# Performance work log

Hardware: AMD Instinct MI355X
Metric: run time of the kernel (lower is better)

The kernel has to match this reference:

```python
import jax, jax.numpy as jnp
import numpy as np

N_EMBEDS = 1024
N_HEADS = 16
HEAD_DIM = N_EMBEDS // N_HEADS
SCALE = HEAD_DIM ** (-0.5)
B, T = 2, 2048


def setup_inputs() -> dict:
    key = jax.random.key(0)
    k1, k2, k3, k4 = jax.random.split(key, 4)
    x = jax.random.normal(k1, (B, T, N_EMBEDS), dtype=jnp.float32)
    # Glorot-uniform-style init like keras Dense defaults (scale irrelevant for correctness)
    w_qkv = jax.random.normal(k2, (N_EMBEDS, 3 * N_EMBEDS), dtype=jnp.float32) * (N_EMBEDS ** -0.5)
    w_proj = jax.random.normal(k3, (N_EMBEDS, N_EMBEDS), dtype=jnp.float32) * (N_EMBEDS ** -0.5)
    b_proj = jnp.zeros((N_EMBEDS,), dtype=jnp.float32)
    return {"x": x, "w_qkv": w_qkv, "w_proj": w_proj, "b_proj": b_proj}


def reference(x, w_qkv, w_proj, b_proj):
    Bc, Tc, D = x.shape
    qkv = x @ w_qkv                                   # [B,T,3D]
    q, k, v = jnp.split(qkv, 3, axis=-1)
    def heads(t):
        return t.reshape(Bc, Tc, N_HEADS, HEAD_DIM).transpose(0, 2, 1, 3)  # [B,H,T,hd]
    q, k, v = heads(q), heads(k), heads(v)
    att = jnp.einsum("bhqd,bhkd->bhqk", q, k) * SCALE  # [B,H,T,T]
    causal = jnp.tril(jnp.ones((Tc, Tc), dtype=bool))[None, None]
    att = jnp.where(causal, att, jnp.float32(-1e9))
    att = jax.nn.softmax(att, axis=-1)
    out = jnp.einsum("bhqk,bhkd->bhqd", att, v)        # [B,H,T,hd]
    out = out.transpose(0, 2, 1, 3).reshape(Bc, Tc, D)
    return out @ w_proj + b_proj
```

## Files before the change

### kernel.cpp

```cpp
#include <hip/hip_runtime.h>
#include <hip/hip_bf16.h>


typedef __bf16 bf16;
typedef float f32x4 __attribute__((ext_vector_type(4)));
typedef float f32x16 __attribute__((ext_vector_type(16)));
typedef bf16 bf16x4 __attribute__((ext_vector_type(4)));
typedef bf16 bf16x8 __attribute__((ext_vector_type(8)));

#define B_ 2
#define T_ 2048
#define D_ 1024
#define H_ 16
#define HD_ 64
#define QSPLIT 9

__device__ __forceinline__ f32x16 mfma32(bf16x8 a, bf16x8 b, f32x16 c) {
    return __builtin_amdgcn_mfma_f32_32x32x16_bf16(a, b, c, 0, 0, 0);
}

__device__ __forceinline__ void gload16(void* l, const void* g) {
    __builtin_amdgcn_global_load_lds(
        (const __attribute__((address_space(1))) unsigned int*)g,
        (__attribute__((address_space(3))) unsigned int*)l, 16, 0, 0);
}

__device__ __forceinline__ f32x16 z16() {
    f32x16 v;
#pragma unroll
    for (int i = 0; i < 16; ++i) v[i] = 0.f;
    return v;
}

__global__ __launch_bounds__(256) void cast_f32_bf16(const float* __restrict__ in,
                                                     bf16* __restrict__ out, int n4) {
    int i = blockIdx.x * 256 + threadIdx.x;
    if (i < n4) {
        float4 v = ((const float4*)in)[i];
        bf16x4 o = { (bf16)v.x, (bf16)v.y, (bf16)v.z, (bf16)v.w };
        ((bf16x4*)out)[i] = o;
    }
}

__global__ __launch_bounds__(256) void cast_transpose(const float* __restrict__ in,
                                                      bf16* __restrict__ out, int R, int C) {
    __shared__ float tile[32][33];
    int cx = blockIdx.x * 32 + threadIdx.x;
    int r0 = blockIdx.y * 32;
#pragma unroll
    for (int j = 0; j < 32; j += 8)
        tile[threadIdx.y + j][threadIdx.x] = in[(size_t)(r0 + threadIdx.y + j) * C + cx];
    __syncthreads();
    int rx = r0 + threadIdx.x;
    int c0 = blockIdx.x * 32;
#pragma unroll
    for (int j = 0; j < 32; j += 8)
        out[(size_t)(c0 + threadIdx.y + j) * R + rx] = (bf16)tile[threadIdx.x][threadIdx.y + j];
}

__global__ __launch_bounds__(256) void transpose_v(const bf16* __restrict__ vb,
                                                   bf16* __restrict__ vt) {
    __shared__ bf16 st[64 * 65];
    const int bh = blockIdx.y;
    const int t0 = blockIdx.x * 64;
    const int tid = threadIdx.x;
#pragma unroll
    for (int c = 0; c < 2; ++c) {
        int cid = tid + c * 256;
        int r = cid >> 3, col = (cid & 7) * 8;
        bf16x8 v = *(const bf16x8*)&vb[((size_t)bh * T_ + t0 + r) * HD_ + col];
#pragma unroll
        for (int j = 0; j < 8; ++j) st[r * 65 + col + j] = v[j];
    }
    __syncthreads();
#pragma unroll
    for (int c = 0; c < 2; ++c) {
        int cid = tid + c * 256;
        int tg = cid & 7, d = cid >> 3;
        bf16x8 o;
#pragma unroll
        for (int j = 0; j < 8; ++j) o[j] = st[(tg * 8 + j) * 65 + d];
        *(bf16x8*)&vt[((size_t)bh * HD_ + d) * T_ + t0 + tg * 8] = o;
    }
}

template <int MW, int NWN, int EPI>
__global__ __launch_bounds__(256) void gemm_k(
    const bf16* __restrict__ A, const bf16* __restrict__ Bt,
    int M, int N, int K,
    bf16* __restrict__ qb, bf16* __restrict__ kb, bf16* __restrict__ vb,
    const float* __restrict__ bias, float* __restrict__ outf) {
    constexpr int BM = 64 * MW;
    constexpr int BN = 64 * NWN;
    __shared__ bf16 sA[BM * 64];
    __shared__ bf16 sB[BN * 64];
    const int tid = threadIdx.x;
    const int wave = tid >> 6, lane = tid & 63;
    const int ln = lane & 31, hi = lane >> 5;
    const int wr = (wave >> 1) * (32 * MW);
    const int wc = (wave & 1) * (32 * NWN);
    const int m0 = blockIdx.x * BM, n0 = blockIdx.y * BN;

    f32x16 acc[MW][NWN];
#pragma unroll
    for (int mi = 0; mi < MW; ++mi)
#pragma unroll
        for (int ni = 0; ni < NWN; ++ni) acc[mi][ni] = z16();

    for (int k0 = 0; k0 < K; k0 += 64) {
        __syncthreads();
#pragma unroll
        for (int j = 0; j < 2 * MW; ++j) {
            int c = tid + 256 * j;
            int r = c >> 3, g = (c & 7) ^ (r & 7);
            gload16(&sA[c * 8], A + (size_t)(m0 + r) * K + k0 + 8 * g);
        }
#pragma unroll
        for (int j = 0; j < 2 * NWN; ++j) {
            int c = tid + 256 * j;
            int r = c >> 3, g = (c & 7) ^ (r & 7);
            gload16(&sB[c * 8], Bt + (size_t)(n0 + r) * K + k0 + 8 * g);
        }
        __syncthreads();
#pragma unroll
        for (int s = 0; s < 4; ++s) {
            bf16x8 av[MW], bv[NWN];
#pragma unroll
            for (int mi = 0; mi < MW; ++mi) {
                int r = wr + mi * 32 + ln;
                av[mi] = *(const bf16x8*)((const char*)sA + r * 128 +
                                          ((((s << 1) | hi) ^ (r & 7)) << 4));
            }
#pragma unroll
            for (int ni = 0; ni < NWN; ++ni) {
                int r = wc + ni * 32 + ln;
                bv[ni] = *(const bf16x8*)((const char*)sB + r * 128 +
                                          ((((s << 1) | hi) ^ (r & 7)) << 4));
            }
#pragma unroll
            for (int mi = 0; mi < MW; ++mi)
#pragma unroll
                for (int ni = 0; ni < NWN; ++ni)
                    acc[mi][ni] = mfma32(av[mi], bv[ni], acc[mi][ni]);
        }
    }

#pragma unroll
    for (int mi = 0; mi < MW; ++mi)
#pragma unroll
        for (int ni = 0; ni < NWN; ++ni)
#pragma unroll
            for (int r = 0; r < 16; ++r) {
                int row = m0 + wr + mi * 32 + (r & 3) + 8 * (r >> 2) + 4 * hi;
                int col = n0 + wc + ni * 32 + ln;
                float v = acc[mi][ni][r];
                if (EPI == 0) {
                    int part = col >> 10, h = (col >> 6) & 15, d = col & 63;
                    int b = row >> 11, t = row & (T_ - 1);
                    size_t idx = ((size_t)(b * H_ + h) * T_ + t) * HD_ + d;
                    bf16* dst = (part == 0) ? qb : (part == 1) ? kb : vb;
                    dst[idx] = (bf16)v;
                } else {
                    outf[(size_t)row * N + col] = v + bias[col];
                }
            }
}

__device__ __forceinline__ bf16x8 kread(const char* base, int row, int s, int hi) {
    int b = (row * 128 + s * 32 + hi * 16) ^ ((row & 7) << 4);
    return *(const bf16x8*)(base + b);
}
__device__ __forceinline__ bf16x8 vread(const char* base, int row, int s, int hi) {
    int sw = (row & 7) << 4;
    int b0 = (row * 128 + s * 32 + hi * 8) ^ sw;
    int b1 = (row * 128 + s * 32 + hi * 8 + 16) ^ sw;
    bf16x4 lo = *(const bf16x4*)(base + b0);
    bf16x4 hi4 = *(const bf16x4*)(base + b1);
    return __builtin_shufflevector(lo, hi4, 0, 1, 2, 3, 4, 5, 6, 7);
}

__global__ __launch_bounds__(256, 3) void attn_kernel(
    const bf16* __restrict__ qb, const bf16* __restrict__ kb,
    const bf16* __restrict__ vtb, bf16* __restrict__ ob,
    bf16* __restrict__ oP, float2* __restrict__ mlP) {
    __shared__ bf16 sK2[2][4096];
    __shared__ bf16 sV2[2][4096];

    const int bid = blockIdx.x;
    const int bh = bid & 31;
    const int sid = bid >> 5;
    int qt, seg, t0, t1;
    if (sid < QSPLIT) {
        qt = sid; seg = -1; t0 = 0; t1 = 2 * qt + 2;
    } else {
        int idx = sid - QSPLIT;
        qt = QSPLIT + (idx >> 1);
        seg = idx & 1;
        if (seg == 0) { t0 = 0; t1 = qt + 1; }
        else          { t0 = qt + 1; t1 = 2 * qt + 2; }
    }
    const int b = bh >> 4, h = bh & 15;
    const int tid = threadIdx.x, wave = tid >> 6, lane = tid & 63;
    const int ln = lane & 31, hi = lane >> 5;
    const int qs = qt * 128 + wave * 32;
    const int qrow = qs + ln;

    const bf16* Qg = qb + (size_t)bh * (T_ * HD_);
    const bf16* Kg = kb + (size_t)bh * (T_ * HD_);
    const bf16* Vtg = vtb + (size_t)bh * (HD_ * T_);

    bf16x8 qf[4];
#pragma unroll
    for (int s = 0; s < 4; ++s) {
        bf16x8 v = *(const bf16x8*)&Qg[(size_t)qrow * HD_ + s * 16 + hi * 8];
#pragma unroll
        for (int e = 0; e < 8; ++e) v[e] = (bf16)((float)v[e] * 0.1803368801f);
        qf[s] = v;
    }
    bf16x8 ones;
#pragma unroll
    for (int e = 0; e < 8; ++e) ones[e] = (bf16)1.0f;

    const int rr0 = tid >> 3;
    const int gg = ((tid & 7) ^ (rr0 & 7)) * 8;

    {
        int kv0 = t0 * 64;
        gload16(&sK2[0][tid * 8], Kg + (size_t)(kv0 + rr0) * HD_ + gg);
        gload16(&sK2[0][(tid + 256) * 8], Kg + (size_t)(kv0 + rr0 + 32) * HD_ + gg);
        gload16(&sV2[0][tid * 8], Vtg + (size_t)rr0 * T_ + kv0 + gg);
        gload16(&sV2[0][(tid + 256) * 8], Vtg + (size_t)(rr0 + 32) * T_ + kv0 + gg);
    }
    __syncthreads();

    const float NINF = -__builtin_inff();
    f32x16 oA = z16(), oB = z16();
    float mR = NINF, lR = 0.f;
    int cur = 0;

    for (int t = t0; t < t1; ++t) {
        if ((t + 1) < t1) {
            int kv0 = (t + 1) * 64;
            bf16* kd = sK2[cur ^ 1];
            bf16* vd = sV2[cur ^ 1];
            gload16(&kd[tid * 8], Kg + (size_t)(kv0 + rr0) * HD_ + gg);
            gload16(&kd[(tid + 256) * 8], Kg + (size_t)(kv0 + rr0 + 32) * HD_ + gg);
            gload16(&vd[tid * 8], Vtg + (size_t)rr0 * T_ + kv0 + gg);
            gload16(&vd[(tid + 256) * 8], Vtg + (size_t)(rr0 + 32) * T_ + kv0 + gg);
        }

        if (64 * t <= qs + 31) {
            const char* kbase = (const char*)sK2[cur];
            const char* vbase = (const char*)sV2[cur];

            f32x16 p0 = z16(), p1 = z16();
            __builtin_amdgcn_s_setprio(1);
#pragma unroll
            for (int s = 0; s < 4; ++s) {
                bf16x8 a0 = kread(kbase, ln, s, hi);
                bf16x8 a1 = kread(kbase, ln + 32, s, hi);
                p0 = mfma32(a0, qf[s], p0);
                p1 = mfma32(a1, qf[s], p1);
            }
            __builtin_amdgcn_s_setprio(0);

            if (64 * t + 63 > qs) {
                int kvb = 64 * t + 4 * hi;
#pragma unroll
                for (int r = 0; r < 16; ++r) {
                    int kvr = kvb + (r & 3) + 8 * (r >> 2);
                    if (kvr > qrow) p0[r] = NINF;
                    if (kvr + 32 > qrow) p1[r] = NINF;
                }
            }

            float mx0 = NINF, mx1 = NINF, mx2 = NINF, mx3 = NINF;
#pragma unroll
            for (int r = 0; r < 16; r += 4) {
                mx0 = fmaxf(fmaxf(p0[r], p1[r]), mx0);
                mx1 = fmaxf(fmaxf(p0[r + 1], p1[r + 1]), mx1);
                mx2 = fmaxf(fmaxf(p0[r + 2], p1[r + 2]), mx2);
                mx3 = fmaxf(fmaxf(p0[r + 3], p1[r + 3]), mx3);
            }
            float pm = fmaxf(fmaxf(mx0, mx1), fmaxf(mx2, mx3));
            pm = fmaxf(pm, __shfl_xor(pm, 32));

            if (__any(pm > mR + 8.f)) {
                float mnew = fmaxf(mR, pm);
                float fac = exp2f(mR - mnew);
                lR *= fac;
#pragma unroll
                for (int r = 0; r < 16; ++r) { oA[r] *= fac; oB[r] *= fac; }
                mR = mnew;
            }

            bf16x8 pa0, pa1, pa2, pa3;
#pragma unroll
            for (int e = 0; e < 8; ++e) {
                pa0[e] = (bf16)exp2f(p0[e] - mR);
                pa1[e] = (bf16)exp2f(p0[8 + e] - mR);
                pa2[e] = (bf16)exp2f(p1[e] - mR);
                pa3[e] = (bf16)exp2f(p1[8 + e] - mR);
            }

            __builtin_amdgcn_s_setprio(1);
            f32x16 sacc = mfma32(ones, pa0, z16());
            sacc = mfma32(ones, pa1, sacc);
            sacc = mfma32(ones, pa2, sacc);
            sacc = mfma32(ones, pa3, sacc);
#pragma unroll
            for (int s = 0; s < 4; ++s) {
                bf16x8 pas = (s == 0) ? pa0 : (s == 1) ? pa1 : (s == 2) ? pa2 : pa3;
                oA = mfma32(vread(vbase, ln, s, hi), pas, oA);
                oB = mfma32(vread(vbase, ln + 32, s, hi), pas, oB);
            }
            __builtin_amdgcn_s_setprio(0);
            lR += sacc[0];
        }

        __syncthreads();
        cur ^= 1;
    }

    if (seg < 0) {
        float inv = 1.f / lR;
        bf16* orow = ob + ((size_t)(b * T_ + qrow)) * D_ + h * HD_;
#pragma unroll
        for (int g = 0; g < 4; ++g) {
            bf16x4 w, w2;
#pragma unroll
            for (int j = 0; j < 4; ++j) {
                w[j] = (bf16)(oA[4 * g + j] * inv);
                w2[j] = (bf16)(oB[4 * g + j] * inv);
            }
            *(bf16x4*)&orow[4 * hi + 8 * g] = w;
            *(bf16x4*)&orow[32 + 4 * hi + 8 * g] = w2;
        }
    } else {
        int row = wave * 32 + ln;
        size_t sbase = (((size_t)bh * (16 - QSPLIT) + (qt - QSPLIT)) * 2 + seg);
        bf16* prow = oP + (sbase * 128 + row) * 64;
#pragma unroll
        for (int g = 0; g < 4; ++g) {
            bf16x4 w, w2;
#pragma unroll
            for (int j = 0; j < 4; ++j) {
                w[j] = (bf16)oA[4 * g + j];
                w2[j] = (bf16)oB[4 * g + j];
            }
            *(bf16x4*)&prow[4 * hi + 8 * g] = w;
            *(bf16x4*)&prow[32 + 4 * hi + 8 * g] = w2;
        }
        if (hi == 0) mlP[sbase * 128 + row] = make_float2(mR, lR);
    }
}

__global__ __launch_bounds__(256) void attn_merge(
    const bf16* __restrict__ oP, const float2* __restrict__ mlP,
    bf16* __restrict__ ob) {
    constexpr int NQS = 16 - QSPLIT;
    int gid = blockIdx.x * 256 + threadIdx.x;
    int bh = gid / (NQS * 128);
    int rem = gid - bh * (NQS * 128);
    int qi = rem >> 7, row = rem & 127;
    int b = bh >> 4, h = bh & 15;
    int t = (QSPLIT + qi) * 128 + row;
    size_t sbase = ((size_t)bh * NQS + qi) * 2;
    float2 ml0 = mlP[(sbase + 0) * 128 + row];
    float2 ml1 = mlP[(sbase + 1) * 128 + row];
    float ms = fmaxf(ml0.x, ml1.x);
    float w0 = exp2f(ml0.x - ms), w1 = exp2f(ml1.x - ms);
    float inv = 1.f / (ml0.y * w0 + ml1.y * w1);
    w0 *= inv; w1 *= inv;
    const bf16* r0 = oP + ((sbase + 0) * 128 + row) * 64;
    const bf16* r1 = oP + ((sbase + 1) * 128 + row) * 64;
    bf16* dst = ob + ((size_t)(b * T_ + t)) * D_ + h * HD_;
#pragma unroll
    for (int g = 0; g < 8; ++g) {
        bf16x8 a = *(const bf16x8*)&r0[g * 8];
        bf16x8 c = *(const bf16x8*)&r1[g * 8];
        bf16x8 o;
#pragma unroll
        for (int j = 0; j < 8; ++j)
            o[j] = (bf16)((float)a[j] * w0 + (float)c[j] * w1);
        *(bf16x8*)&dst[g * 8] = o;
    }
}

extern "C" void kernel_launch(void* const* d_in, const int* in_sizes, int n_in,
                              void* d_out, int out_size, void* d_ws, size_t ws_size,
                              hipStream_t stream) {
    const float* x = (const float*)d_in[0];
    const float* w_qkv = (const float*)d_in[1];
    const float* w_proj = (const float*)d_in[2];
    const float* b_proj = (const float*)d_in[3];
    float* out = (float*)d_out;
    char* ws = (char*)d_ws;

    bf16* xb = (bf16*)(ws);
    bf16* ob = (bf16*)(ws);
    bf16* wqkvt = (bf16*)(ws + 8388608);
    bf16* vtbuf = (bf16*)(ws + 8388608);
    bf16* qbuf = (bf16*)(ws + 16777216);
    bf16* wprojt = (bf16*)(ws + 16777216);
    bf16* kbuf = (bf16*)(ws + 25165824);
    bf16* vbuf = (bf16*)(ws + 33554432);
    bf16* oP = (bf16*)(ws + 33554432);
    float2* mlP = (float2*)(ws + 33554432 + 7340032);

    cast_f32_bf16<<<4096, 256, 0, stream>>>(x, xb, (B_ * T_ * D_) / 4);
    dim3 tb(32, 8);
    cast_transpose<<<dim3(3 * D_ / 32, D_ / 32), tb, 0, stream>>>(w_qkv, wqkvt, D_, 3 * D_);

    gemm_k<2, 2, 0><<<dim3((B_ * T_) / 128, (3 * D_) / 128), 256, 0, stream>>>(
        xb, wqkvt, B_ * T_, 3 * D_, D_, qbuf, kbuf, vbuf, nullptr, nullptr);

    transpose_v<<<dim3(T_ / 64, B_ * H_), 256, 0, stream>>>(vbuf, vtbuf);

    attn_kernel<<<23 * 32, 256, 0, stream>>>(qbuf, kbuf, vtbuf, ob, oP, mlP);
    attn_merge<<<112, 256, 0, stream>>>(oP, mlP, ob);

    cast_transpose<<<dim3(D_ / 32, D_ / 32), tb, 0, stream>>>(w_proj, wprojt, D_, D_);

    gemm_k<1, 2, 1><<<dim3((B_ * T_) / 64, D_ / 128), 256, 0, stream>>>(
        ob, wprojt, B_ * T_, D_, D_, nullptr, nullptr, nullptr, b_proj, out);
}
```

Baseline: 123.8 us.

## Triple-buffer K/V tiles and overlap next-tile QK^T with current softmax/PV

Replaces the double-buffered attention loop with a three-stage LDS ring. Loads for tile t+2 are issued while the QK^T MFMAs for tile t+1 run alongside the softmax and PV work of tile t, with the loop unrolled by two so the score registers alternate. The goal is to hide LDS and global-load latency and keep the MFMA units busy, at the cost of more LDS and registers, so occupancy drops from 3 to 2 blocks per CU. The per-wave causal skip of fully masked tiles is dropped, adding some wasted work. The row-max cross-half shuffle now happens only inside the rescale branch, so the two lane halves can hold different running maxima. That is reconciled only for the split-segment outputs, which is a correctness risk.

Measured after the change: 131.9 us. +6.6%, slower.

```diff
diff --git a/kernel.cpp b/kernel.cpp
--- a/kernel.cpp
+++ b/kernel.cpp
@@ -179,12 +179,12 @@
     return __builtin_shufflevector(lo, hi4, 0, 1, 2, 3, 4, 5, 6, 7);
 }
 
-__global__ __launch_bounds__(256, 3) void attn_kernel(
+__global__ __launch_bounds__(256, 2) void attn_kernel(
     const bf16* __restrict__ qb, const bf16* __restrict__ kb,
     const bf16* __restrict__ vtb, bf16* __restrict__ ob,
     bf16* __restrict__ oP, float2* __restrict__ mlP) {
-    __shared__ bf16 sK2[2][4096];
-    __shared__ bf16 sV2[2][4096];
+    __shared__ bf16 sK3[3][4096];
+    __shared__ bf16 sV3[3][4096];
 
     const int bid = blockIdx.x;
     const int bh = bid & 31;
@@ -224,102 +224,118 @@
     const int rr0 = tid >> 3;
     const int gg = ((tid & 7) ^ (rr0 & 7)) * 8;
 
-    {
-        int kv0 = t0 * 64;
-        gload16(&sK2[0][tid * 8], Kg + (size_t)(kv0 + rr0) * HD_ + gg);
-        gload16(&sK2[0][(tid + 256) * 8], Kg + (size_t)(kv0 + rr0 + 32) * HD_ + gg);
-        gload16(&sV2[0][tid * 8], Vtg + (size_t)rr0 * T_ + kv0 + gg);
-        gload16(&sV2[0][(tid + 256) * 8], Vtg + (size_t)(rr0 + 32) * T_ + kv0 + gg);
-    }
-    __syncthreads();
+#define STAGE(T, BUF)                                                           \
+    do {                                                                        \
+        int kv0_ = (T) * 64;                                                    \
+        gload16(&sK3[BUF][tid * 8], Kg + (size_t)(kv0_ + rr0) * HD_ + gg);      \
+        gload16(&sK3[BUF][(tid + 256) * 8],                                     \
+                Kg + (size_t)(kv0_ + rr0 + 32) * HD_ + gg);                     \
+        gload16(&sV3[BUF][tid * 8], Vtg + (size_t)rr0 * T_ + kv0_ + gg);        \
+        gload16(&sV3[BUF][(tid + 256) * 8],                                     \
+                Vtg + (size_t)(rr0 + 32) * T_ + kv0_ + gg);                     \
+    } while (0)
+
+#define QK_STEP(BUFK, PN0, PN1)                                                 \
+    do {                                                                        \
+        const char* kbase_ = (const char*)sK3[BUFK];                            \
+        f32x16 q0_ = z16(), q1_ = z16();                                        \
+        __builtin_amdgcn_s_setprio(1);                                          \
+        _Pragma("unroll") for (int s_ = 0; s_ < 4; ++s_) {                      \
+            q0_ = mfma32(kread(kbase_, ln, s_, hi), qf[s_], q0_);               \
+            q1_ = mfma32(kread(kbase_, ln + 32, s_, hi), qf[s_], q1_);          \
+        }                                                                       \
+        __builtin_amdgcn_s_setprio(0);                                          \
+        PN0 = q0_;                                                              \
+        PN1 = q1_;                                                              \
+    } while (0)
+
+#define SM_PV(T, PC0, PC1)                                                      \
+    do {                                                                        \
+        if (64 * (T) + 63 > qs) {        \
+            int kvb_ = 64 * (T) + 4 * hi;                                       \
+            _Pragma("unroll") for (int r_ = 0; r_ < 16; ++r_) {                 \
+                int kvr_ = kvb_ + (r_ & 3) + 8 * (r_ >> 2);                     \
+                if (kvr_ > qrow) PC0[r_] = NINF;                                \
+                if (kvr_ + 32 > qrow) PC1[r_] = NINF;                           \
+            }                                                                   \
+        }                                                                       \
+        float mx0_ = NINF, mx1_ = NINF, mx2_ = NINF, mx3_ = NINF;               \
+        _Pragma("unroll") for (int r_ = 0; r_ < 16; r_ += 4) {                  \
+            mx0_ = fmaxf(fmaxf(PC0[r_], PC1[r_]), mx0_);                        \
+            mx1_ = fmaxf(fmaxf(PC0[r_ + 1], PC1[r_ + 1]), mx1_);                \
+            mx2_ = fmaxf(fmaxf(PC0[r_ + 2], PC1[r_ + 2]), mx2_);                \
+            mx3_ = fmaxf(fmaxf(PC0[r_ + 3], PC1[r_ + 3]), mx3_);                \
+        }                                                                       \
+        float pm_ = fmaxf(fmaxf(mx0_, mx1_), fmaxf(mx2_, mx3_));                \
+         \
+                        \
+        if (__any(pm_ > mR + 8.f)) {                                            \
+            float pmw_ = fmaxf(pm_, __shfl_xor(pm_, 32));                       \
+            float mnew_ = fmaxf(mR, pmw_);                                      \
+            float fac_ = exp2f(mR - mnew_);                                     \
+            lR *= fac_;                                                         \
+            _Pragma("unroll") for (int r_ = 0; r_ < 16; ++r_) {                 \
+                oA[r_] *= fac_;                                                 \
+                oB[r_] *= fac_;                                                 \
+            }                                                                   \
+            mR = mnew_;                                                         \
+        }                                                                       \
+        bf16x8 pa0_, pa1_, pa2_, pa3_;                                          \
+        _Pragma("unroll") for (int e_ = 0; e_ < 8; ++e_) {                      \
+            pa0_[e_] = (bf16)exp2f(PC0[e_] - mR);                               \
+            pa1_[e_] = (bf16)exp2f(PC0[8 + e_] - mR);                           \
+            pa2_[e_] = (bf16)exp2f(PC1[e_] - mR);                               \
+            pa3_[e_] = (bf16)exp2f(PC1[8 + e_] - mR);                           \
+        }                                                                       \
+        const char* vbase_ = (const char*)sV3[bA];                              \
+        __builtin_amdgcn_s_setprio(1);                                          \
+        f32x16 sacc_ = mfma32(ones, pa0_, z16());                               \
+        sacc_ = mfma32(ones, pa1_, sacc_);                                      \
+        sacc_ = mfma32(ones, pa2_, sacc_);                                      \
+        sacc_ = mfma32(ones, pa3_, sacc_);                                      \
+        oA = mfma32(vread(vbase_, ln, 0, hi), pa0_, oA);                        \
+        oB = mfma32(vread(vbase_, ln + 32, 0, hi), pa0_, oB);                   \
+        oA = mfma32(vread(vbase_, ln, 1, hi), pa1_, oA);                        \
+        oB = mfma32(vread(vbase_, ln + 32, 1, hi), pa1_, oB);                   \
+        oA = mfma32(vread(vbase_, ln, 2, hi), pa2_, oA);                        \
+        oB = mfma32(vread(vbase_, ln + 32, 2, hi), pa2_, oB);                   \
+        oA = mfma32(vread(vbase_, ln, 3, hi), pa3_, oA);                        \
+        oB = mfma32(vread(vbase_, ln + 32, 3, hi), pa3_, oB);                   \
+        __builtin_amdgcn_s_setprio(0);                                          \
+        lR += sacc_[0];                                                         \
+    } while (0)
+
+#define BODY(T, PC0, PC1, PN0, PN1)                                             \
+    do {                                                                        \
+        if ((T) + 2 < t1) STAGE((T) + 2, bC);                                   \
+        if ((T) + 1 < t1) QK_STEP(bB, PN0, PN1);                                \
+        SM_PV(T, PC0, PC1);                                                     \
+        __syncthreads();                                                        \
+        int tmp_ = bA;                                                          \
+        bA = bB;                                                                \
+        bB = bC;                                                                \
+        bC = tmp_;                                                              \
+    } while (0)
 
     const float NINF = -__builtin_inff();
     f32x16 oA = z16(), oB = z16();
     float mR = NINF, lR = 0.f;
-    int cur = 0;
-
-    for (int t = t0; t < t1; ++t) {
-        if ((t + 1) < t1) {
-            int kv0 = (t + 1) * 64;
-            bf16* kd = sK2[cur ^ 1];
-            bf16* vd = sV2[cur ^ 1];
-            gload16(&kd[tid * 8], Kg + (size_t)(kv0 + rr0) * HD_ + gg);
-            gload16(&kd[(tid + 256) * 8], Kg + (size_t)(kv0 + rr0 + 32) * HD_ + gg);
-            gload16(&vd[tid * 8], Vtg + (size_t)rr0 * T_ + kv0 + gg);
-            gload16(&vd[(tid + 256) * 8], Vtg + (size_t)(rr0 + 32) * T_ + kv0 + gg);
-        }
-
-        if (64 * t <= qs + 31) {
-            const char* kbase = (const char*)sK2[cur];
-            const char* vbase = (const char*)sV2[cur];
-
-            f32x16 p0 = z16(), p1 = z16();
-            __builtin_amdgcn_s_setprio(1);
-#pragma unroll
-            for (int s = 0; s < 4; ++s) {
-                bf16x8 a0 = kread(kbase, ln, s, hi);
-                bf16x8 a1 = kread(kbase, ln + 32, s, hi);
-                p0 = mfma32(a0, qf[s], p0);
-                p1 = mfma32(a1, qf[s], p1);
-            }
-            __builtin_amdgcn_s_setprio(0);
-
-            if (64 * t + 63 > qs) {
-                int kvb = 64 * t + 4 * hi;
-#pragma unroll
-                for (int r = 0; r < 16; ++r) {
-                    int kvr = kvb + (r & 3) + 8 * (r >> 2);
-                    if (kvr > qrow) p0[r] = NINF;
-                    if (kvr + 32 > qrow) p1[r] = NINF;
-                }
-            }
-
-            float mx0 = NINF, mx1 = NINF, mx2 = NINF, mx3 = NINF;
-#pragma unroll
-            for (int r = 0; r < 16; r += 4) {
-                mx0 = fmaxf(fmaxf(p0[r], p1[r]), mx0);
-                mx1 = fmaxf(fmaxf(p0[r + 1], p1[r + 1]), mx1);
-                mx2 = fmaxf(fmaxf(p0[r + 2], p1[r + 2]), mx2);
-                mx3 = fmaxf(fmaxf(p0[r + 3], p1[r + 3]), mx3);
-            }
-            float pm = fmaxf(fmaxf(mx0, mx1), fmaxf(mx2, mx3));
-            pm = fmaxf(pm, __shfl_xor(pm, 32));
-
-            if (__any(pm > mR + 8.f)) {
-                float mnew = fmaxf(mR, pm);
-                float fac = exp2f(mR - mnew);
-                lR *= fac;
-#pragma unroll
-                for (int r = 0; r < 16; ++r) { oA[r] *= fac; oB[r] *= fac; }
-                mR = mnew;
-            }
-
-            bf16x8 pa0, pa1, pa2, pa3;
-#pragma unroll
-            for (int e = 0; e < 8; ++e) {
-                pa0[e] = (bf16)exp2f(p0[e] - mR);
-                pa1[e] = (bf16)exp2f(p0[8 + e] - mR);
-                pa2[e] = (bf16)exp2f(p1[e] - mR);
-                pa3[e] = (bf16)exp2f(p1[8 + e] - mR);
-            }
-
-            __builtin_amdgcn_s_setprio(1);
-            f32x16 sacc = mfma32(ones, pa0, z16());
-            sacc = mfma32(ones, pa1, sacc);
-            sacc = mfma32(ones, pa2, sacc);
-            sacc = mfma32(ones, pa3, sacc);
-#pragma unroll
-            for (int s = 0; s < 4; ++s) {
-                bf16x8 pas = (s == 0) ? pa0 : (s == 1) ? pa1 : (s == 2) ? pa2 : pa3;
-                oA = mfma32(vread(vbase, ln, s, hi), pas, oA);
-                oB = mfma32(vread(vbase, ln + 32, s, hi), pas, oB);
-            }
-            __builtin_amdgcn_s_setprio(0);
-            lR += sacc[0];
-        }
-
-        __syncthreads();
-        cur ^= 1;
+    int bA = 0, bB = 1, bC = 2;
+
+    STAGE(t0, 0);
+    __syncthreads();
+    if (t0 + 1 < t1) STAGE(t0 + 1, 1);
+    f32x16 pE0, pE1, pO0, pO1;
+    QK_STEP(0, pE0, pE1);
+    __syncthreads();
+
+    int t = t0;
+    for (; t + 1 < t1; t += 2) {
+        BODY(t, pE0, pE1, pO0, pO1);
+        BODY(t + 1, pO0, pO1, pE0, pE1);
+    }
+    if (t < t1) {
+        BODY(t, pE0, pE1, pO0, pO1);
     }
 
     if (seg < 0) {
@@ -337,6 +353,14 @@
             *(bf16x4*)&orow[32 + 4 * hi + 8 * g] = w2;
         }
     } else {
+        float mW = fmaxf(mR, __shfl_xor(mR, 32));
+        if (mW != mR) {
+            float fac = exp2f(mR - mW);
+            lR *= fac;
+#pragma unroll
+            for (int r = 0; r < 16; ++r) { oA[r] *= fac; oB[r] *= fac; }
+            mR = mW;
+        }
         int row = wave * 32 + ln;
         size_t sbase = (((size_t)bh * (16 - QSPLIT) + (qt - QSPLIT)) * 2 + seg);
         bf16* prow = oP + (sbase * 128 + row) * 64;
@@ -353,6 +377,10 @@
         }
         if (hi == 0) mlP[sbase * 128 + row] = make_float2(mR, lR);
     }
+#undef STAGE
+#undef QK_STEP
+#undef SM_PV
+#undef BODY
 }
 
 __global__ __launch_bounds__(256) void attn_merge(
```

## Triple-buffer K/V tiles in LDS with partial vmcnt waits

Applied to the files above, without the earlier changes.

Moves the K/V shared-memory staging from double to triple buffering, so loads for tile t+2 are issued while tile t is computed. The full __syncthreads is replaced by an explicit s_waitcnt vmcnt(4) plus s_barrier, letting the newest tile's loads stay in flight across the barrier. The goal is to hide more global-load latency in the attention loop. In exchange, LDS per block grows from 32 KB to 48 KB, which could limit occupancy, and correctness now depends on the hand-counted vmcnt values.

After: 126.5 us. 2.1% more time.

```diff
diff --git a/kernel.cpp b/kernel.cpp
--- a/kernel.cpp
+++ b/kernel.cpp
@@ -183,8 +183,8 @@
     const bf16* __restrict__ qb, const bf16* __restrict__ kb,
     const bf16* __restrict__ vtb, bf16* __restrict__ ob,
     bf16* __restrict__ oP, float2* __restrict__ mlP) {
-    __shared__ bf16 sK2[2][4096];
-    __shared__ bf16 sV2[2][4096];
+    __shared__ bf16 sK3[3][4096];
+    __shared__ bf16 sV3[3][4096];
 
     const int bid = blockIdx.x;
     const int bh = bid & 31;
@@ -224,34 +224,39 @@
     const int rr0 = tid >> 3;
     const int gg = ((tid & 7) ^ (rr0 & 7)) * 8;
 
-    {
-        int kv0 = t0 * 64;
-        gload16(&sK2[0][tid * 8], Kg + (size_t)(kv0 + rr0) * HD_ + gg);
-        gload16(&sK2[0][(tid + 256) * 8], Kg + (size_t)(kv0 + rr0 + 32) * HD_ + gg);
-        gload16(&sV2[0][tid * 8], Vtg + (size_t)rr0 * T_ + kv0 + gg);
-        gload16(&sV2[0][(tid + 256) * 8], Vtg + (size_t)(rr0 + 32) * T_ + kv0 + gg);
-    }
-    __syncthreads();
+#define STAGE(T, BUF)                                                           \
+    do {                                                                        \
+        int kv0_ = (T) * 64;                                                    \
+        gload16(&sK3[BUF][tid * 8], Kg + (size_t)(kv0_ + rr0) * HD_ + gg);      \
+        gload16(&sK3[BUF][(tid + 256) * 8],                                     \
+                Kg + (size_t)(kv0_ + rr0 + 32) * HD_ + gg);                     \
+        gload16(&sV3[BUF][tid * 8], Vtg + (size_t)rr0 * T_ + kv0_ + gg);        \
+        gload16(&sV3[BUF][(tid + 256) * 8],                                     \
+                Vtg + (size_t)(rr0 + 32) * T_ + kv0_ + gg);                     \
+    } while (0)
+
+    STAGE(t0, 0);
+    if (t0 + 1 < t1) {
+        STAGE(t0 + 1, 1);
+        asm volatile("s_waitcnt vmcnt(4)" ::: "memory");
+    } else {
+        asm volatile("s_waitcnt vmcnt(0)" ::: "memory");
+    }
+    __builtin_amdgcn_sched_barrier(0);
+    __builtin_amdgcn_s_barrier();
+    __builtin_amdgcn_sched_barrier(0);
 
     const float NINF = -__builtin_inff();
     f32x16 oA = z16(), oB = z16();
     float mR = NINF, lR = 0.f;
-    int cur = 0;
+    int bA = 0, bB = 1, bC = 2;
 
     for (int t = t0; t < t1; ++t) {
-        if ((t + 1) < t1) {
-            int kv0 = (t + 1) * 64;
-            bf16* kd = sK2[cur ^ 1];
-            bf16* vd = sV2[cur ^ 1];
-            gload16(&kd[tid * 8], Kg + (size_t)(kv0 + rr0) * HD_ + gg);
-            gload16(&kd[(tid + 256) * 8], Kg + (size_t)(kv0 + rr0 + 32) * HD_ + gg);
-            gload16(&vd[tid * 8], Vtg + (size_t)rr0 * T_ + kv0 + gg);
-            gload16(&vd[(tid + 256) * 8], Vtg + (size_t)(rr0 + 32) * T_ + kv0 + gg);
-        }
+        if (t + 2 < t1) STAGE(t + 2, bC);
 
         if (64 * t <= qs + 31) {
-            const char* kbase = (const char*)sK2[cur];
-            const char* vbase = (const char*)sV2[cur];
+            const char* kbase = (const char*)sK3[bA];
+            const char* vbase = (const char*)sV3[bA];
 
             f32x16 p0 = z16(), p1 = z16();
             __builtin_amdgcn_s_setprio(1);
@@ -318,9 +323,19 @@
             lR += sacc[0];
         }
 
-        __syncthreads();
-        cur ^= 1;
-    }
+        if (t + 1 < t1) {
+            if (t + 2 < t1) {
+                asm volatile("s_waitcnt vmcnt(4)" ::: "memory");
+            } else {
+                asm volatile("s_waitcnt vmcnt(0)" ::: "memory");
+            }
+            __builtin_amdgcn_sched_barrier(0);
+            __builtin_amdgcn_s_barrier();
+            __builtin_amdgcn_sched_barrier(0);
+        }
+        int tmp = bA; bA = bB; bB = bC; bC = tmp;
+    }
+#undef STAGE
 
     if (seg < 0) {
         float inv = 1.f / lR;
```
